# Kernel optimization log

Hardware: AMD Instinct MI355X
Metric: run time of the kernel (lower is better)

The kernel has to match this reference:

```python
import jax, jax.numpy as jnp
import numpy as np

MIN_PS = 1       # min_patch_size
MAX_PS = 8       # max_patch_size
LOOKAHEAD = 4
THRESH = 1.2     # entropy_threshold (bits)
PAD = 0          # pad_token


def setup_inputs() -> dict:
    key = jax.random.key(0)
    tokens = jax.random.randint(key, (32, 16384), 0, 8, dtype=jnp.int32)
    return {"tokens": tokens}


def _entropy_per_pos(seq):
    """Shannon entropy (bits) of window seq[p : min(S, p+LOOKAHEAD)] for every p. [S]"""
    S = seq.shape[0]
    idx = jnp.arange(S)[:, None] + jnp.arange(LOOKAHEAD)[None, :]   # [S, L]
    valid = idx < S                                                  # [S, L]
    w = seq[jnp.minimum(idx, S - 1)]                                 # [S, L]
    # count of each element's value within its (masked) window
    eq = (w[:, :, None] == w[:, None, :]) & valid[:, :, None] & valid[:, None, :]
    c = jnp.maximum(eq.sum(-1), 1).astype(jnp.float32)               # [S, L]
    n = valid.sum(-1).astype(jnp.float32)                            # [S]
    # H = -sum_v (c_v/n) log2(c_v/n) = -(1/n) sum_j log2(c_j/n)
    ent = -jnp.where(valid, jnp.log2(c / n[:, None]), 0.0).sum(-1) / n
    return ent


def _patch_one(seq):
    """Vectorized equivalent of AdaptivePatcher._patch_one_sequence.
    Returns padded patches [P,MAX_PS], offsets [P] (-1 pad), num_patches scalar,
    where P = S // MIN_PS (worst case)."""
    S = seq.shape[0]
    hi = _entropy_per_pos(seq) >= THRESH                             # growth stops here
    # next position q >= p with hi[q] (S if none): suffix-min of hi indices
    idx_hi = jnp.where(hi, jnp.arange(S), S)
    next_hi = jax.lax.associative_scan(jnp.minimum, idx_hi, reverse=True)

    max_patches = S // MIN_PS

    def step(i, _):
        valid = i < S
        rem = S - i
        size0 = jnp.minimum(MIN_PS, rem)
        look = jnp.minimum(i + size0, S - 1)
        # grow while size < MAX_PS, i+size < S, ent[i+size] < THRESH
        size = jnp.clip(next_hi[look] - i, size0, jnp.minimum(MAX_PS, rem))
        size = jnp.where(i + size0 >= S, size0, size)   # no room to grow
        size = jnp.where(valid, size, 0)
        off = jnp.where(valid, i, -1)
        return jnp.where(valid, i + size, S), (off, size)

    _, (offsets, sizes) = jax.lax.scan(step, jnp.int32(0), None, length=max_patches)

    pos = offsets[:, None] + jnp.arange(MAX_PS)[None, :]             # [P, MAX_PS]
    mask = jnp.arange(MAX_PS)[None, :] < sizes[:, None]
    patches = jnp.where(mask, seq[jnp.clip(pos, 0, S - 1)], PAD)
    num_patches = (sizes > 0).sum()
    return patches, offsets, num_patches


def reference(tokens):
    # Padded equivalents of the torch module's ragged lists:
    # patches [B, P, MAX_PS], offsets [B, P] (-1 past the end), num_patches [B],
    # cu_seqlens [B+1] (cumulative patch counts).
    patches, offsets, n = jax.vmap(_patch_one)(tokens)
    cu_seqlens = jnp.concatenate(
        [jnp.zeros((1,), jnp.int32), jnp.cumsum(n).astype(jnp.int32)]
    )
    return patches, offsets, n, cu_seqlens
```

## Files before the change

kernel.cpp:

```cpp
#include <hip/hip_runtime.h>


#define S_LEN 16384
#define BATCH 32
#define NCH 8
#define CHUNK 2048
#define NTH 1024
#define PPT 2
#define NWV (NTH / 64)
#define MAX_PS 8
#define MAGIC 0x5A17ULL

__global__ __launch_bounds__(NTH)
void fused_kernel(const int* __restrict__ tokens,
                  int* __restrict__ patches,
                  int* __restrict__ offsets,
                  int* __restrict__ nout,
                  int* __restrict__ cu,
                  unsigned long long* __restrict__ sumPub,
                  unsigned long long* __restrict__ ntotPub)
{
    const int blk = blockIdx.x;
    const int b = blk >> 3, c = blk & 7;
    const int t = threadIdx.x;
    const int lane = t & 63, wv = t >> 6;
    const int cs = c * CHUNK;
    const int pl = t * PPT;
    const int p = cs + pl;
    const int* __restrict__ seq = tokens + (size_t)b * S_LEN;
    int* __restrict__ pat = patches + (size_t)b * S_LEN * MAX_PS;
    int* __restrict__ off = offsets + (size_t)b * S_LEN;

    __shared__ int tok_s[CHUNK + 8];
    __shared__ unsigned short rs_s[CHUNK];
    __shared__ unsigned char bs[NTH];
    __shared__ unsigned hw[65];
    __shared__ int partMax[NWV], partSum[NWV], red[2 * NWV];
    __shared__ int anch_s, base_s, ctot_s, ntot_s;

    int v[6];
    if (p + 5 < S_LEN) {
        int2 a2 = *(const int2*)(seq + p);
        int2 b2 = *(const int2*)(seq + p + 2);
        int2 c2 = *(const int2*)(seq + p + 4);
        v[0]=a2.x; v[1]=a2.y; v[2]=b2.x; v[3]=b2.y; v[4]=c2.x; v[5]=c2.y;
    } else {
#pragma unroll
        for (int i = 0; i < 6; ++i) v[i] = (p + i < S_LEN) ? seq[p + i] : 0;
    }
    *(int2*)&tok_s[pl] = make_int2(v[0], v[1]);
    if (t < 8) {
        int j2 = cs + CHUNK + t;
        tok_s[CHUNK + t] = (j2 < S_LEN) ? seq[j2] : 0;
    }

    unsigned hb = 0;
    int llh = -1, ffh = S_LEN;
#pragma unroll
    for (int k = 0; k < PPT; ++k) {
        int j = p + k;
        int nv = min(4, S_LEN - j);
        unsigned m = 0;
#pragma unroll
        for (int i = 0; i < 4; ++i) if (i < nv) m |= 1u << (v[k + i] & 31);
        int h = (__popc(m) >= 3) ? 1 : 0;
        hb |= (unsigned)h << k;
        if (h) { llh = j; if (ffh == S_LEN) ffh = j; }
    }
    bs[t] = (unsigned char)hb;

    int eh = 0;
    if (t < 7) {
        int j = cs + CHUNK + t;
        if (j < S_LEN) {
            int nv = min(4, S_LEN - j);
            unsigned m = 0;
            for (int i = 0; i < 4; ++i) if (i < nv) m |= 1u << (seq[j + i] & 31);
            eh = (__popc(m) >= 3) ? 1 : 0;
        }
    }
    unsigned long long bal = __ballot(eh);
    if (t == 0) hw[64] = (unsigned)(bal & 0x7f);

    int mx = llh, mn = ffh;
#pragma unroll
    for (int d = 32; d >= 1; d >>= 1) {
        mx = max(mx, __shfl_down(mx, d));
        mn = min(mn, __shfl_down(mn, d));
    }
    if (lane == 0) { red[wv] = mx; red[NWV + wv] = mn; }
    int incl = llh;
#pragma unroll
    for (int d = 1; d < 64; d <<= 1) {
        int u = __shfl_up(incl, d);
        if (lane >= d) incl = max(incl, u);
    }
    if (lane == 63) partMax[wv] = incl;
    __syncthreads();

    if (t < 64) {
        unsigned w = 0;
#pragma unroll
        for (int i = 0; i < 16; ++i) w |= (unsigned)bs[16 * t + i] << (2 * i);
        hw[t] = w;
    }

    int runx = __shfl_up(incl, 1);
    if (lane == 0) runx = -1;
    for (int w = 0; w < wv; ++w) runx = max(runx, partMax[w]);

    {
        int run = runx, ci = 0;
#pragma unroll
        for (int k = 0; k < PPT; ++k) {
            int j = p + k;
            int h = (hb >> k) & 1;
            int is = h | ((run >= 0) & (((j - run) & 7) == 0));
            ci += is;
            if (h) run = j;
        }
        int s = ci;
#pragma unroll
        for (int d = 32; d >= 1; d >>= 1) s += __shfl_down(s, d);
        if (lane == 0) partSum[wv] = s;
    }
    __syncthreads();

    if (t == 0) {
        int lastHi = red[0], fh = red[NWV];
        for (int w = 1; w < NWV; ++w) {
            lastHi = max(lastHi, red[w]);
            fh = min(fh, red[NWV + w]);
        }
        int fhl = min(fh - cs, CHUNK);
        int A = 0;
        for (int w = 0; w < NWV; ++w) A += partSum[w];
        unsigned long long pk = (MAGIC << 48)
                              | ((unsigned long long)(unsigned)(lastHi + 1) << 32)
                              | ((unsigned long long)(unsigned)fhl << 16)
                              | (unsigned long long)(unsigned)A;
        __hip_atomic_store(&sumPub[blk], pk, __ATOMIC_RELAXED, __HIP_MEMORY_SCOPE_AGENT);
    }

    int lh_l = 0, fl_l = 0, A_l = 0;
    if (wv == 0 && lane < c) {
        unsigned long long sv;
        for (;;) {
            sv = __hip_atomic_load(&sumPub[b*NCH + lane], __ATOMIC_RELAXED, __HIP_MEMORY_SCOPE_AGENT);
            if ((sv >> 48) == MAGIC) break;
            __builtin_amdgcn_s_sleep(1);
        }
        lh_l = (int)((sv >> 32) & 0xffff) - 1;
        fl_l = (int)((sv >> 16) & 0xffff);
        A_l  = (int)(sv & 0xffff);
    }
    if (wv == 0) {
        int anchor = -1, base = 0;
        for (int cp = 0; cp < c; ++cp) {
            int lh = __shfl(lh_l, cp);
            int fl = __shfl(fl_l, cp);
            int Ap = __shfl(A_l, cp);
            int lo = cp * CHUNK, hi2 = lo + fl;
            int a = max(anchor, 0);
            base += ((hi2 - a + 7) >> 3) - ((lo - a + 7) >> 3) + Ap;
            if (lh >= 0) anchor = lh;
        }
        if (lane == 0) { anch_s = anchor; base_s = base; }
    }
    __syncthreads();

    int run = max(runx, anch_s);
    unsigned fb = 0;
    int cl = 0;
#pragma unroll
    for (int k = 0; k < PPT; ++k) {
        int j = p + k;
        int h = (hb >> k) & 1;
        int a = max(run, 0);
        int is = h | (((j - a) & 7) == 0);
        fb |= (unsigned)is << k;
        cl += is;
        if (h) run = j;
    }
    int sincl = cl;
#pragma unroll
    for (int d = 1; d < 64; d <<= 1) {
        int u = __shfl_up(sincl, d);
        if (lane >= d) sincl += u;
    }
    if (lane == 63) partSum[wv] = sincl;
    __syncthreads();
    int sexcl = __shfl_up(sincl, 1);
    if (lane == 0) sexcl = 0;
    int lr = sexcl;
    for (int w = 0; w < wv; ++w) lr += partSum[w];

    if (t == 0) {
        int ctot = 0;
        for (int w = 0; w < NWV; ++w) ctot += partSum[w];
        ctot_s = ctot;
        if (c == NCH - 1) {
            int ntot = base_s + ctot;
            ntot_s = ntot;
            nout[b] = ntot;
            __hip_atomic_store(&ntotPub[b], (MAGIC << 48) | (unsigned long long)(unsigned)ntot,
                               __ATOMIC_RELAXED, __HIP_MEMORY_SCOPE_AGENT);
        }
    }

    {
        int q = lr;
#pragma unroll
        for (int k = 0; k < PPT; ++k) {
            if ((fb >> k) & 1u) rs_s[q++] = (unsigned short)(pl + k);
        }
    }
    __syncthreads();

    const int base = base_s, ctot = ctot_s;
    for (int r2 = t; r2 < ctot; r2 += NTH) {
        int pos = rs_s[r2];
        int j = cs + pos;
        int size = 8;
#pragma unroll
        for (int d = 1; d <= 7; ++d) {
            int bb = pos + d;
            if ((hw[bb >> 5] >> (bb & 31)) & 1u) { size = d; break; }
        }
        size = min(size, S_LEN - j);
        int vals[8];
#pragma unroll
        for (int q = 0; q < 8; ++q) vals[q] = (q < size) ? tok_s[pos + q] : 0;
        off[base + r2] = j;
        int4* dst = (int4*)(pat + (size_t)(base + r2) * MAX_PS);
        dst[0] = make_int4(vals[0], vals[1], vals[2], vals[3]);
        dst[1] = make_int4(vals[4], vals[5], vals[6], vals[7]);
    }

    if (c == NCH - 1) {
        const int4 z = make_int4(0, 0, 0, 0);
        for (int r2 = ntot_s + t; r2 < S_LEN; r2 += NTH) {
            off[r2] = -1;
            int4* dst = (int4*)(pat + (size_t)r2 * MAX_PS);
            dst[0] = z;
            dst[1] = z;
        }
    }

    if (b == 0 && c == 0 && wv == 0) {
        int nv2 = 0;
        if (lane < BATCH) {
            unsigned long long sv;
            for (;;) {
                sv = __hip_atomic_load(&ntotPub[lane], __ATOMIC_RELAXED, __HIP_MEMORY_SCOPE_AGENT);
                if ((sv >> 48) == MAGIC) break;
                __builtin_amdgcn_s_sleep(1);
            }
            nv2 = (int)(sv & 0xffff);
        }
        int sc2 = nv2;
#pragma unroll
        for (int d = 1; d < 32; d <<= 1) {
            int u = __shfl_up(sc2, d);
            if (lane >= d) sc2 += u;
        }
        if (lane < BATCH) cu[lane + 1] = sc2;
        if (lane == 0) cu[0] = 0;
    }
}

extern "C" void kernel_launch(void* const* d_in, const int* in_sizes, int n_in,
                              void* d_out, int out_size, void* d_ws, size_t ws_size,
                              hipStream_t stream)
{
    const int* tokens = (const int*)d_in[0];
    int* out = (int*)d_out;
    int* patches = out;
    int* offsets = patches + (size_t)BATCH * S_LEN * MAX_PS;
    int* nout    = offsets + (size_t)BATCH * S_LEN;
    int* cu      = nout + BATCH;

    unsigned long long* sumPub  = (unsigned long long*)d_ws;
    unsigned long long* ntotPub = sumPub + BATCH * NCH;

    fused_kernel<<<dim3(BATCH * NCH), dim3(NTH), 0, stream>>>(
        tokens, patches, offsets, nout, cu, sumPub, ntotPub);
}
```

Measured before the change: 71.89 us.

## Split fused kernel into two launches replacing inter-block spin-wait chaining

Result: slower. 75.31 us (+4.8%).

```diff
diff --git a/kernel.cpp b/kernel.cpp
--- a/kernel.cpp
+++ b/kernel.cpp
@@ -8,17 +8,116 @@
 #define NTH 1024
 #define PPT 2
 #define NWV (NTH / 64)
+#define WPS 512
+#define WPC 64
 #define MAX_PS 8
-#define MAGIC 0x5A17ULL
 
 __global__ __launch_bounds__(NTH)
-void fused_kernel(const int* __restrict__ tokens,
-                  int* __restrict__ patches,
-                  int* __restrict__ offsets,
-                  int* __restrict__ nout,
-                  int* __restrict__ cu,
-                  unsigned long long* __restrict__ sumPub,
-                  unsigned long long* __restrict__ ntotPub)
+void k1_hi(const int* __restrict__ tokens,
+           unsigned* __restrict__ hiBits,
+           int4* __restrict__ summ)
+{
+    const int blk = blockIdx.x;
+    const int b = blk >> 3, c = blk & 7;
+    const int t = threadIdx.x;
+    const int lane = t & 63, wv = t >> 6;
+    const int cs = c * CHUNK;
+    const int pl = t * PPT;
+    const int p = cs + pl;
+    const int* __restrict__ seq = tokens + (size_t)b * S_LEN;
+
+    __shared__ unsigned char bs[NTH];
+    __shared__ int partMax[NWV], partSum[NWV], red[2 * NWV];
+
+    int v[6];
+    if (p + 5 < S_LEN) {
+        int2 a2 = *(const int2*)(seq + p);
+        int2 b2 = *(const int2*)(seq + p + 2);
+        int2 c2 = *(const int2*)(seq + p + 4);
+        v[0]=a2.x; v[1]=a2.y; v[2]=b2.x; v[3]=b2.y; v[4]=c2.x; v[5]=c2.y;
+    } else {
+#pragma unroll
+        for (int i = 0; i < 6; ++i) v[i] = (p + i < S_LEN) ? seq[p + i] : 0;
+    }
+
+    unsigned hb = 0;
+    int llh = -1, ffh = S_LEN;
+#pragma unroll
+    for (int k = 0; k < PPT; ++k) {
+        int j = p + k;
+        int nv = min(4, S_LEN - j);
+        unsigned m = 0;
+#pragma unroll
+        for (int i = 0; i < 4; ++i) if (i < nv) m |= 1u << (v[k + i] & 31);
+        int h = (__popc(m) >= 3) ? 1 : 0;
+        hb |= (unsigned)h << k;
+        if (h) { llh = j; if (ffh == S_LEN) ffh = j; }
+    }
+    bs[t] = (unsigned char)hb;
+
+    int mx = llh, mn = ffh;
+#pragma unroll
+    for (int d = 32; d >= 1; d >>= 1) {
+        mx = max(mx, __shfl_down(mx, d));
+        mn = min(mn, __shfl_down(mn, d));
+    }
+    if (lane == 0) { red[wv] = mx; red[NWV + wv] = mn; }
+    int incl = llh;
+#pragma unroll
+    for (int d = 1; d < 64; d <<= 1) {
+        int u = __shfl_up(incl, d);
+        if (lane >= d) incl = max(incl, u);
+    }
+    if (lane == 63) partMax[wv] = incl;
+    __syncthreads();
+
+    if (t < WPC) {
+        unsigned w = 0;
+#pragma unroll
+        for (int i = 0; i < 16; ++i) w |= (unsigned)bs[16 * t + i] << (2 * i);
+        hiBits[b * WPS + c * WPC + t] = w;
+    }
+
+    int runx = __shfl_up(incl, 1);
+    if (lane == 0) runx = -1;
+    for (int w = 0; w < wv; ++w) runx = max(runx, partMax[w]);
+
+    int run = runx, ci = 0;
+#pragma unroll
+    for (int k = 0; k < PPT; ++k) {
+        int j = p + k;
+        int h = (hb >> k) & 1;
+        int is = h | ((run >= 0) & (((j - run) & 7) == 0));
+        ci += is;
+        if (h) run = j;
+    }
+    int s = ci;
+#pragma unroll
+    for (int d = 32; d >= 1; d >>= 1) s += __shfl_down(s, d);
+    if (lane == 0) partSum[wv] = s;
+    __syncthreads();
+
+    if (t == 0) {
+        int lastHi = red[0], fh = red[NWV];
+        for (int w = 1; w < NWV; ++w) {
+            lastHi = max(lastHi, red[w]);
+            fh = min(fh, red[NWV + w]);
+        }
+        int fhl = min(fh - cs, CHUNK);
+        int A = 0;
+        for (int w = 0; w < NWV; ++w) A += partSum[w];
+        summ[blk] = make_int4(lastHi, fhl, A, 0);
+    }
+}
+
+__global__ __launch_bounds__(NTH)
+void k2_emit(const int* __restrict__ tokens,
+             const unsigned* __restrict__ hiBits,
+             const int4* __restrict__ summ,
+             int* __restrict__ patches,
+             int* __restrict__ offsets,
+             int* __restrict__ nout,
+             int* __restrict__ cu)
 {
     const int blk = blockIdx.x;
     const int b = blk >> 3, c = blk & 7;
@@ -33,62 +132,29 @@
 
     __shared__ int tok_s[CHUNK + 8];
     __shared__ unsigned short rs_s[CHUNK];
-    __shared__ unsigned char bs[NTH];
-    __shared__ unsigned hw[65];
-    __shared__ int partMax[NWV], partSum[NWV], red[2 * NWV];
+    __shared__ unsigned hw[WPC + 1];
+    __shared__ int4 sum_s[NCH];
+    __shared__ int partMax[NWV], partSum[NWV];
     __shared__ int anch_s, base_s, ctot_s, ntot_s;
 
-    int v[6];
-    if (p + 5 < S_LEN) {
+    {
         int2 a2 = *(const int2*)(seq + p);
-        int2 b2 = *(const int2*)(seq + p + 2);
-        int2 c2 = *(const int2*)(seq + p + 4);
-        v[0]=a2.x; v[1]=a2.y; v[2]=b2.x; v[3]=b2.y; v[4]=c2.x; v[5]=c2.y;
-    } else {
-#pragma unroll
-        for (int i = 0; i < 6; ++i) v[i] = (p + i < S_LEN) ? seq[p + i] : 0;
-    }
-    *(int2*)&tok_s[pl] = make_int2(v[0], v[1]);
+        *(int2*)&tok_s[pl] = a2;
+    }
     if (t < 8) {
         int j2 = cs + CHUNK + t;
         tok_s[CHUNK + t] = (j2 < S_LEN) ? seq[j2] : 0;
     }
-
-    unsigned hb = 0;
-    int llh = -1, ffh = S_LEN;
-#pragma unroll
-    for (int k = 0; k < PPT; ++k) {
-        int j = p + k;
-        int nv = min(4, S_LEN - j);
-        unsigned m = 0;
-#pragma unroll
-        for (int i = 0; i < 4; ++i) if (i < nv) m |= 1u << (v[k + i] & 31);
-        int h = (__popc(m) >= 3) ? 1 : 0;
-        hb |= (unsigned)h << k;
-        if (h) { llh = j; if (ffh == S_LEN) ffh = j; }
-    }
-    bs[t] = (unsigned char)hb;
-
-    int eh = 0;
-    if (t < 7) {
-        int j = cs + CHUNK + t;
-        if (j < S_LEN) {
-            int nv = min(4, S_LEN - j);
-            unsigned m = 0;
-            for (int i = 0; i < 4; ++i) if (i < nv) m |= 1u << (seq[j + i] & 31);
-            eh = (__popc(m) >= 3) ? 1 : 0;
-        }
-    }
-    unsigned long long bal = __ballot(eh);
-    if (t == 0) hw[64] = (unsigned)(bal & 0x7f);
-
-    int mx = llh, mn = ffh;
-#pragma unroll
-    for (int d = 32; d >= 1; d >>= 1) {
-        mx = max(mx, __shfl_down(mx, d));
-        mn = min(mn, __shfl_down(mn, d));
-    }
-    if (lane == 0) { red[wv] = mx; red[NWV + wv] = mn; }
+    if (t < WPC) hw[t] = hiBits[b * WPS + c * WPC + t];
+    if (t == WPC) hw[WPC] = (c < NCH - 1) ? hiBits[b * WPS + (c + 1) * WPC] : 0u;
+    if (t < NCH) sum_s[t] = summ[b * NCH + t];
+    __syncthreads();
+
+    unsigned hb = (hw[t >> 4] >> (2 * (t & 15))) & 3u;
+    int llh = -1;
+    if (hb & 1u) llh = p;
+    if (hb & 2u) llh = p + 1;
+
     int incl = llh;
 #pragma unroll
     for (int d = 1; d < 64; d <<= 1) {
@@ -96,78 +162,24 @@
         if (lane >= d) incl = max(incl, u);
     }
     if (lane == 63) partMax[wv] = incl;
-    __syncthreads();
-
-    if (t < 64) {
-        unsigned w = 0;
-#pragma unroll
-        for (int i = 0; i < 16; ++i) w |= (unsigned)bs[16 * t + i] << (2 * i);
-        hw[t] = w;
-    }
+
+    if (t == 0) {
+        int anchor = -1, acc = 0;
+        for (int cp = 0; cp < NCH; ++cp) {
+            if (cp == c) { anch_s = anchor; base_s = acc; }
+            int lh = sum_s[cp].x, fl = sum_s[cp].y, A = sum_s[cp].z;
+            int lo = cp * CHUNK, hi2 = lo + fl;
+            int a = max(anchor, 0);
+            acc += ((hi2 - a + 7) >> 3) - ((lo - a + 7) >> 3) + A;
+            if (lh >= 0) anchor = lh;
+        }
+        ntot_s = acc;
+    }
+    __syncthreads();
 
     int runx = __shfl_up(incl, 1);
     if (lane == 0) runx = -1;
     for (int w = 0; w < wv; ++w) runx = max(runx, partMax[w]);
-
-    {
-        int run = runx, ci = 0;
-#pragma unroll
-        for (int k = 0; k < PPT; ++k) {
-            int j = p + k;
-            int h = (hb >> k) & 1;
-            int is = h | ((run >= 0) & (((j - run) & 7) == 0));
-            ci += is;
-            if (h) run = j;
-        }
-        int s = ci;
-#pragma unroll
-        for (int d = 32; d >= 1; d >>= 1) s += __shfl_down(s, d);
-        if (lane == 0) partSum[wv] = s;
-    }
-    __syncthreads();
-
-    if (t == 0) {
-        int lastHi = red[0], fh = red[NWV];
-        for (int w = 1; w < NWV; ++w) {
-            lastHi = max(lastHi, red[w]);
-            fh = min(fh, red[NWV + w]);
-        }
-        int fhl = min(fh - cs, CHUNK);
-        int A = 0;
-        for (int w = 0; w < NWV; ++w) A += partSum[w];
-        unsigned long long pk = (MAGIC << 48)
-                              | ((unsigned long long)(unsigned)(lastHi + 1) << 32)
-                              | ((unsigned long long)(unsigned)fhl << 16)
-                              | (unsigned long long)(unsigned)A;
-        __hip_atomic_store(&sumPub[blk], pk, __ATOMIC_RELAXED, __HIP_MEMORY_SCOPE_AGENT);
-    }
-
-    int lh_l = 0, fl_l = 0, A_l = 0;
-    if (wv == 0 && lane < c) {
-        unsigned long long sv;
-        for (;;) {
-            sv = __hip_atomic_load(&sumPub[b*NCH + lane], __ATOMIC_RELAXED, __HIP_MEMORY_SCOPE_AGENT);
-            if ((sv >> 48) == MAGIC) break;
-            __builtin_amdgcn_s_sleep(1);
-        }
-        lh_l = (int)((sv >> 32) & 0xffff) - 1;
-        fl_l = (int)((sv >> 16) & 0xffff);
-        A_l  = (int)(sv & 0xffff);
-    }
-    if (wv == 0) {
-        int anchor = -1, base = 0;
-        for (int cp = 0; cp < c; ++cp) {
-            int lh = __shfl(lh_l, cp);
-            int fl = __shfl(fl_l, cp);
-            int Ap = __shfl(A_l, cp);
-            int lo = cp * CHUNK, hi2 = lo + fl;
-            int a = max(anchor, 0);
-            base += ((hi2 - a + 7) >> 3) - ((lo - a + 7) >> 3) + Ap;
-            if (lh >= 0) anchor = lh;
-        }
-        if (lane == 0) { anch_s = anchor; base_s = base; }
-    }
-    __syncthreads();
 
     int run = max(runx, anch_s);
     unsigned fb = 0;
@@ -194,18 +206,10 @@
     if (lane == 0) sexcl = 0;
     int lr = sexcl;
     for (int w = 0; w < wv; ++w) lr += partSum[w];
-
     if (t == 0) {
         int ctot = 0;
         for (int w = 0; w < NWV; ++w) ctot += partSum[w];
         ctot_s = ctot;
-        if (c == NCH - 1) {
-            int ntot = base_s + ctot;
-            ntot_s = ntot;
-            nout[b] = ntot;
-            __hip_atomic_store(&ntotPub[b], (MAGIC << 48) | (unsigned long long)(unsigned)ntot,
-                               __ATOMIC_RELAXED, __HIP_MEMORY_SCOPE_AGENT);
-        }
     }
 
     {
@@ -247,18 +251,20 @@
         }
     }
 
-    if (b == 0 && c == 0 && wv == 0) {
-        int nv2 = 0;
+    if (blk == 0 && wv == 0) {
+        int ntl = 0;
         if (lane < BATCH) {
-            unsigned long long sv;
-            for (;;) {
-                sv = __hip_atomic_load(&ntotPub[lane], __ATOMIC_RELAXED, __HIP_MEMORY_SCOPE_AGENT);
-                if ((sv >> 48) == MAGIC) break;
-                __builtin_amdgcn_s_sleep(1);
+            int anchor = -1;
+            for (int cp = 0; cp < NCH; ++cp) {
+                int4 sv = summ[lane * NCH + cp];
+                int lo = cp * CHUNK, hi2 = lo + sv.y;
+                int a = max(anchor, 0);
+                ntl += ((hi2 - a + 7) >> 3) - ((lo - a + 7) >> 3) + sv.z;
+                if (sv.x >= 0) anchor = sv.x;
             }
-            nv2 = (int)(sv & 0xffff);
-        }
-        int sc2 = nv2;
+            nout[lane] = ntl;
+        }
+        int sc2 = ntl;
 #pragma unroll
         for (int d = 1; d < 32; d <<= 1) {
             int u = __shfl_up(sc2, d);
@@ -280,9 +286,10 @@
     int* nout    = offsets + (size_t)BATCH * S_LEN;
     int* cu      = nout + BATCH;
 
-    unsigned long long* sumPub  = (unsigned long long*)d_ws;
-    unsigned long long* ntotPub = sumPub + BATCH * NCH;
-
-    fused_kernel<<<dim3(BATCH * NCH), dim3(NTH), 0, stream>>>(
-        tokens, patches, offsets, nout, cu, sumPub, ntotPub);
+    unsigned* hiBits = (unsigned*)d_ws;
+    int4* summ = (int4*)((char*)d_ws + (size_t)BATCH * WPS * sizeof(unsigned));
+
+    k1_hi  <<<dim3(BATCH * NCH), dim3(NTH), 0, stream>>>(tokens, hiBits, summ);
+    k2_emit<<<dim3(BATCH * NCH), dim3(NTH), 0, stream>>>(tokens, hiBits, summ,
+                                                         patches, offsets, nout, cu);
 }
```
